# Performance work log

Measured on AMD Instinct MI355X. Metric: run time of the kernel, lower is better.

The kernel has to match this reference:

```python
import jax, jax.numpy as jnp
import numpy as np

B, H = 65536, 512


def setup_inputs() -> dict:
    key = jax.random.key(0)
    ks = jax.random.split(key, 10)
    s = 1.0 / np.sqrt(H)  # torch nn.Linear default init range
    uni = lambda k, shape: jax.random.uniform(k, shape, jnp.float32, -s, s)
    return {
        "inputs": jax.random.normal(ks[0], (B, H), jnp.float32),
        "short_term_memory": jax.random.normal(ks[1], (B, H), jnp.float32),
        "Wf": uni(ks[2], (H, H)), "bf": uni(ks[3], (H,)),
        "Wi": uni(ks[4], (H, H)), "bi": uni(ks[5], (H,)),
        "Wg": uni(ks[6], (H, H)), "bg": uni(ks[7], (H,)),
        "Wo": uni(ks[8], (H, H)), "bo": uni(ks[9], (H,)),
    }


def reference(inputs, short_term_memory, Wf, bf, Wi, bi, Wg, bg, Wo, bo):
    z = inputs + short_term_memory  # [B, H]
    # ForgetGate: OVERWRITES long-term memory (previous cell state never read).
    c = jax.nn.sigmoid(z @ Wf.T + bf)
    # InputGate: c += sigmoid(...) * tanh(...)
    c = c + jax.nn.sigmoid(z @ Wi.T + bi) * jnp.tanh(z @ Wg.T + bg)
    # OutputGate: h = tanh(c) * sigmoid(...)
    h = jnp.tanh(c) * jax.nn.sigmoid(z @ Wo.T + bo)
    return jnp.stack((c, h))  # [2, B, H]: new long-term and short-term memory
```

## Files before the change

### kernel.cpp

```cpp
#include <hip/hip_runtime.h>

typedef __bf16 bf16x8 __attribute__((ext_vector_type(8)));
typedef float  f32x4  __attribute__((ext_vector_type(4)));

#define LOG2E 1.4426950408889634f

static __device__ __forceinline__ float fexp2(float x) { return __builtin_amdgcn_exp2f(x); }
static __device__ __forceinline__ float frcp(float x)  { return __builtin_amdgcn_rcpf(x); }
static __device__ __forceinline__ float fsigmoid(float x) { return frcp(1.0f + fexp2(-LOG2E * x)); }
static __device__ __forceinline__ float ftanh(float x)    { return 2.0f * frcp(1.0f + fexp2(-2.0f * LOG2E * x)) - 1.0f; }

__global__ __launch_bounds__(256) void wpack(const float* __restrict__ Wf,
                                             const float* __restrict__ Wi,
                                             const float* __restrict__ Wg,
                                             const float* __restrict__ Wo,
                                             __bf16* __restrict__ Wp)
{
    int idx = blockIdx.x * 256 + threadIdx.x;
    int kg  = idx & 63;
    int j   = (idx >> 6) & 511;
    int g   = idx >> 15;
    const float* src = (g == 0) ? Wf : (g == 1) ? Wi : (g == 2) ? Wg : Wo;
    const float4* s4 = (const float4*)(src + j * 512 + kg * 8);
    float4 v0 = s4[0], v1 = s4[1];
    bf16x8 o;
    o[0] = (__bf16)v0.x; o[1] = (__bf16)v0.y; o[2] = (__bf16)v0.z; o[3] = (__bf16)v0.w;
    o[4] = (__bf16)v1.x; o[5] = (__bf16)v1.y; o[6] = (__bf16)v1.z; o[7] = (__bf16)v1.w;
    int cn = j >> 4;
    int ks = kg >> 2;
    int lt = (j & 15) + (kg & 3) * 16;
    size_t dst = ((size_t)(((g * 32 + cn) * 16 + ks) * 64 + lt)) * 8;
    *(bf16x8*)(Wp + dst) = o;
}

__global__ __launch_bounds__(1024, 4) void lstm_main(
    const float* __restrict__ xin, const float* __restrict__ stm,
    const __bf16* __restrict__ Wp,
    const float* __restrict__ bfv, const float* __restrict__ biv,
    const float* __restrict__ bgv, const float* __restrict__ bov,
    float* __restrict__ out)
{
    __shared__ unsigned char zs[131072];
    __shared__ unsigned char xbuf[32768];
    const int tid  = threadIdx.x;
    const int lane = tid & 63;
    const int wv   = tid >> 6;
    const int cn8  = wv & 7;
    const int rh   = wv >> 3;
    const int l15  = lane & 15;
    const int lq   = lane >> 4;
    const int row0 = blockIdx.x * 128;

    {
        const float* xb = xin + (size_t)row0 * 512;
        const float* sb = stm + (size_t)row0 * 512;
        #pragma unroll
        for (int it = 0; it < 8; ++it) {
            int idx = it * 1024 + tid;
            int row = idx >> 6;
            int kg  = idx & 63;
            const float4* x4 = (const float4*)(xb + row * 512 + kg * 8);
            const float4* s4 = (const float4*)(sb + row * 512 + kg * 8);
            float4 a0 = x4[0], a1 = x4[1];
            float4 b0 = s4[0], b1 = s4[1];
            bf16x8 p;
            p[0] = (__bf16)(a0.x + b0.x); p[1] = (__bf16)(a0.y + b0.y);
            p[2] = (__bf16)(a0.z + b0.z); p[3] = (__bf16)(a0.w + b0.w);
            p[4] = (__bf16)(a1.x + b1.x); p[5] = (__bf16)(a1.y + b1.y);
            p[6] = (__bf16)(a1.z + b1.z); p[7] = (__bf16)(a1.w + b1.w);
            int rb   = row >> 5;
            int kk   = kg >> 1;
            int slot = ((row & 31) + (kg & 1) * 32) ^ (kk & 7);
            *(bf16x8*)(zs + rb * 32768 + kk * 1024 + slot * 16) = p;
        }
    }
    __syncthreads();

    const int kkoff = lq >> 1;
    const int s0    = l15 + (lq & 1) * 32;
    const int koffb = kkoff << 10;

    const float* bias_a = rh ? bgv : bfv;
    const float* bias_b = rh ? bov : biv;

    for (int ci = 0; ci < 4; ++ci) {
        const int cn   = ci * 8 + cn8;
        const int colj = cn * 16 + l15;

        const __bf16* bpA = Wp + ((size_t)(((rh * 2    ) * 32 + cn) * 16)) * 512 + lane * 8;
        const __bf16* bpB = Wp + ((size_t)(((rh * 2 + 1) * 32 + cn) * 16)) * 512 + lane * 8;

        float biasA = bias_a[colj], biasB = bias_b[colj];
        f32x4 acc[8][2];
        #pragma unroll
        for (int m = 0; m < 8; ++m) {
            #pragma unroll
            for (int r = 0; r < 4; ++r) { acc[m][0][r] = biasA; acc[m][1][r] = biasB; }
        }

        #pragma unroll 2
        for (int ks = 0; ks < 16; ++ks) {
            const int kk7 = ((2 * ks) & 7) | kkoff;
            const int t0  = ((s0 ^ kk7) << 4) + ks * 2048 + koffb;
            bf16x8 b0 = *(const bf16x8*)(bpA + ks * 512);
            bf16x8 b1 = *(const bf16x8*)(bpB + ks * 512);
            bf16x8 a[8];
            #pragma unroll
            for (int m = 0; m < 8; ++m)
                a[m] = *(const bf16x8*)(zs + (m >> 1) * 32768 + (m & 1) * 256 + t0);
            #pragma unroll
            for (int m = 0; m < 8; ++m) {
                acc[m][0] = __builtin_amdgcn_mfma_f32_16x16x32_bf16(a[m], b0, acc[m][0], 0, 0, 0);
                acc[m][1] = __builtin_amdgcn_mfma_f32_16x16x32_bf16(a[m], b1, acc[m][1], 0, 0, 0);
            }
        }

        unsigned char* wr = xbuf + ((cn8 * 2 + rh) * 2) * 1024 + lane * 16;
        unsigned char* rd = xbuf + ((cn8 * 2 + (1 - rh)) * 2) * 1024 + lane * 16;
        #pragma unroll
        for (int mc = 0; mc < 4; ++mc) {
            __syncthreads();
            if (rh == 0) {
                *(f32x4*)(wr)        = acc[mc + 4][0];
                *(f32x4*)(wr + 1024) = acc[mc + 4][1];
            } else {
                *(f32x4*)(wr)        = acc[mc][0];
                *(f32x4*)(wr + 1024) = acc[mc][1];
            }
            __syncthreads();
            f32x4 t0v = *(const f32x4*)(rd);
            f32x4 t1v = *(const f32x4*)(rd + 1024);
            int mo = rh ? (mc + 4) : mc;
            #pragma unroll
            for (int r = 0; r < 4; ++r) {
                float F, I, G, O;
                if (rh == 0) { F = acc[mc][0][r];     I = acc[mc][1][r];     G = t0v[r]; O = t1v[r]; }
                else         { F = t0v[r]; I = t1v[r]; G = acc[mc + 4][0][r]; O = acc[mc + 4][1][r]; }
                float c = fsigmoid(F) + fsigmoid(I) * ftanh(G);
                float h = ftanh(c) * fsigmoid(O);
                int row = row0 + mo * 16 + lq * 4 + r;
                int o   = row * 512 + colj;
                out[o] = c;
                out[33554432 + o] = h;
            }
        }
    }
}

extern "C" void kernel_launch(void* const* d_in, const int* in_sizes, int n_in,
                              void* d_out, int out_size, void* d_ws, size_t ws_size,
                              hipStream_t stream) {
    const float* xin = (const float*)d_in[0];
    const float* stm = (const float*)d_in[1];
    const float* Wf  = (const float*)d_in[2];
    const float* bf_ = (const float*)d_in[3];
    const float* Wi  = (const float*)d_in[4];
    const float* bi_ = (const float*)d_in[5];
    const float* Wg  = (const float*)d_in[6];
    const float* bg_ = (const float*)d_in[7];
    const float* Wo  = (const float*)d_in[8];
    const float* bo_ = (const float*)d_in[9];
    __bf16* Wp = (__bf16*)d_ws;

    wpack<<<512, 256, 0, stream>>>(Wf, Wi, Wg, Wo, Wp);
    lstm_main<<<512, 1024, 0, stream>>>(xin, stm, Wp, bf_, bi_, bg_, bo_, (float*)d_out);
}
```

Before: 219.8 us.

## Replace block barriers with pairwise LDS flag handoff between gate-half wavefronts

Block-wide __syncthreads in the epilogue exchange are replaced by per-wave-pair producer/consumer flags in LDS. The rh=1 waves hand their G/O accumulators to the rh=0 partner through a single slot, and only rh=0 waves run the activations and stores. The packed weight layout is interleaved by gate so each wave's two B fragments sit close together, and s_setprio is raised around the MFMA block. The aim is to cut barrier stalls and let pairs progress independently, at the cost of spin-wait overhead, an unbalanced epilogue that now runs on half the waves, and subtle memory-ordering risk.

```diff
diff --git a/kernel.cpp b/kernel.cpp
--- a/kernel.cpp
+++ b/kernel.cpp
@@ -29,7 +29,7 @@
     int cn = j >> 4;
     int ks = kg >> 2;
     int lt = (j & 15) + (kg & 3) * 16;
-    size_t dst = ((size_t)(((g * 32 + cn) * 16 + ks) * 64 + lt)) * 8;
+    size_t dst = ((size_t)(((cn * 16 + ks) * 4 + g) * 64 + lt)) * 8;
     *(bf16x8*)(Wp + dst) = o;
 }
 
@@ -41,15 +41,19 @@
     float* __restrict__ out)
 {
     __shared__ unsigned char zs[131072];
-    __shared__ unsigned char xbuf[32768];
+    __shared__ unsigned char xslot[8][2048];
+    __shared__ int pf[8];
+    __shared__ int ackf[8];
     const int tid  = threadIdx.x;
     const int lane = tid & 63;
     const int wv   = tid >> 6;
-    const int cn8  = wv & 7;
+    const int p8   = wv & 7;
     const int rh   = wv >> 3;
     const int l15  = lane & 15;
     const int lq   = lane >> 4;
     const int row0 = blockIdx.x * 128;
+
+    if (tid < 8) { pf[tid] = 0; ackf[tid] = 0; }
 
     {
         const float* xb = xin + (size_t)row0 * 512;
@@ -80,17 +84,17 @@
     const int s0    = l15 + (lq & 1) * 32;
     const int koffb = kkoff << 10;
 
-    const float* bias_a = rh ? bgv : bfv;
-    const float* bias_b = rh ? bov : biv;
+    volatile int* vpf  = (volatile int*)&pf[p8];
+    volatile int* vack = (volatile int*)&ackf[p8];
+    unsigned char* slotb = &xslot[p8][0] + lane * 32;
 
     for (int ci = 0; ci < 4; ++ci) {
-        const int cn   = ci * 8 + cn8;
+        const int cn   = ci * 8 + p8;
         const int colj = cn * 16 + l15;
+        const char* wpB = (const char*)Wp + (size_t)cn * 65536 + rh * 2048 + (size_t)lane * 16;
 
-        const __bf16* bpA = Wp + ((size_t)(((rh * 2    ) * 32 + cn) * 16)) * 512 + lane * 8;
-        const __bf16* bpB = Wp + ((size_t)(((rh * 2 + 1) * 32 + cn) * 16)) * 512 + lane * 8;
-
-        float biasA = bias_a[colj], biasB = bias_b[colj];
+        float biasA = (rh ? bgv : bfv)[colj];
+        float biasB = (rh ? bov : biv)[colj];
         f32x4 acc[8][2];
         #pragma unroll
         for (int m = 0; m < 8; ++m) {
@@ -102,46 +106,52 @@
         for (int ks = 0; ks < 16; ++ks) {
             const int kk7 = ((2 * ks) & 7) | kkoff;
             const int t0  = ((s0 ^ kk7) << 4) + ks * 2048 + koffb;
-            bf16x8 b0 = *(const bf16x8*)(bpA + ks * 512);
-            bf16x8 b1 = *(const bf16x8*)(bpB + ks * 512);
+            bf16x8 b0 = *(const bf16x8*)(wpB + ks * 4096);
+            bf16x8 b1 = *(const bf16x8*)(wpB + ks * 4096 + 1024);
             bf16x8 a[8];
             #pragma unroll
             for (int m = 0; m < 8; ++m)
                 a[m] = *(const bf16x8*)(zs + (m >> 1) * 32768 + (m & 1) * 256 + t0);
+            __builtin_amdgcn_s_setprio(1);
             #pragma unroll
             for (int m = 0; m < 8; ++m) {
                 acc[m][0] = __builtin_amdgcn_mfma_f32_16x16x32_bf16(a[m], b0, acc[m][0], 0, 0, 0);
                 acc[m][1] = __builtin_amdgcn_mfma_f32_16x16x32_bf16(a[m], b1, acc[m][1], 0, 0, 0);
             }
+            __builtin_amdgcn_s_setprio(0);
         }
 
-        unsigned char* wr = xbuf + ((cn8 * 2 + rh) * 2) * 1024 + lane * 16;
-        unsigned char* rd = xbuf + ((cn8 * 2 + (1 - rh)) * 2) * 1024 + lane * 16;
-        #pragma unroll
-        for (int mc = 0; mc < 4; ++mc) {
-            __syncthreads();
-            if (rh == 0) {
-                *(f32x4*)(wr)        = acc[mc + 4][0];
-                *(f32x4*)(wr + 1024) = acc[mc + 4][1];
-            } else {
-                *(f32x4*)(wr)        = acc[mc][0];
-                *(f32x4*)(wr + 1024) = acc[mc][1];
+        if (rh == 1) {
+            #pragma unroll 1
+            for (int m = 0; m < 8; ++m) {
+                const int seq = ci * 8 + m + 1;
+                while (*vack < seq - 1) __builtin_amdgcn_s_sleep(1);
+                asm volatile("" ::: "memory");
+                *(f32x4*)(slotb)      = acc[m][0];
+                *(f32x4*)(slotb + 16) = acc[m][1];
+                asm volatile("s_waitcnt lgkmcnt(0)" ::: "memory");
+                if (lane == 0) *vpf = seq;
             }
-            __syncthreads();
-            f32x4 t0v = *(const f32x4*)(rd);
-            f32x4 t1v = *(const f32x4*)(rd + 1024);
-            int mo = rh ? (mc + 4) : mc;
-            #pragma unroll
-            for (int r = 0; r < 4; ++r) {
-                float F, I, G, O;
-                if (rh == 0) { F = acc[mc][0][r];     I = acc[mc][1][r];     G = t0v[r]; O = t1v[r]; }
-                else         { F = t0v[r]; I = t1v[r]; G = acc[mc + 4][0][r]; O = acc[mc + 4][1][r]; }
-                float c = fsigmoid(F) + fsigmoid(I) * ftanh(G);
-                float h = ftanh(c) * fsigmoid(O);
-                int row = row0 + mo * 16 + lq * 4 + r;
-                int o   = row * 512 + colj;
-                out[o] = c;
-                out[33554432 + o] = h;
+        } else {
+            #pragma unroll 1
+            for (int m = 0; m < 8; ++m) {
+                const int seq = ci * 8 + m + 1;
+                while (*vpf < seq) __builtin_amdgcn_s_sleep(1);
+                asm volatile("" ::: "memory");
+                __builtin_amdgcn_sched_barrier(0);
+                f32x4 vG = *(const f32x4*)(slotb);
+                f32x4 vO = *(const f32x4*)(slotb + 16);
+                asm volatile("s_waitcnt lgkmcnt(0)" ::: "memory");
+                if (lane == 0) *vack = seq;
+                #pragma unroll
+                for (int r = 0; r < 4; ++r) {
+                    float c = fsigmoid(acc[m][0][r]) + fsigmoid(acc[m][1][r]) * ftanh(vG[r]);
+                    float h = ftanh(c) * fsigmoid(vO[r]);
+                    int row = row0 + m * 16 + lq * 4 + r;
+                    int o   = row * 512 + colj;
+                    out[o] = c;
+                    out[33554432 + o] = h;
+                }
             }
         }
     }
```

Result: slower. 370.1 us (+68.4%).

## Software-pipeline weight loads with triple-buffered inline asm and interleaved packed layout

Applied to the files above, without the earlier changes.

Repacks the bf16 weights so that all four gates' fragments for a given column tile and k-step sit next to each other, letting each wave fetch both of its B fragments with one base address. The k-loop is fully unrolled with a three-deep register rotation of global loads issued in inline asm, gated by explicit vmcnt waits, so weight fetches overlap the MFMA work. LDS A reads are split into two halves, and MFMA groups are wrapped in setprio. The aim is to hide global load latency that previously stalled the MFMA chain. The cost is extra VGPR pressure from the buffers and fragile hand-written waitcnt sequencing.

```diff
diff --git a/kernel.cpp b/kernel.cpp
--- a/kernel.cpp
+++ b/kernel.cpp
@@ -29,7 +29,7 @@
     int cn = j >> 4;
     int ks = kg >> 2;
     int lt = (j & 15) + (kg & 3) * 16;
-    size_t dst = ((size_t)(((g * 32 + cn) * 16 + ks) * 64 + lt)) * 8;
+    size_t dst = ((size_t)(((cn * 16 + ks) * 4 + g) * 64 + lt)) * 8;
     *(bf16x8*)(Wp + dst) = o;
 }
 
@@ -45,7 +45,7 @@
     const int tid  = threadIdx.x;
     const int lane = tid & 63;
     const int wv   = tid >> 6;
-    const int cn8  = wv & 7;
+    const int p8   = wv & 7;
     const int rh   = wv >> 3;
     const int l15  = lane & 15;
     const int lq   = lane >> 4;
@@ -77,18 +77,65 @@
     __syncthreads();
 
     const int kkoff = lq >> 1;
-    const int s0    = l15 + (lq & 1) * 32;
+    const int sl0   = l15 + (lq & 1) * 32;
     const int koffb = kkoff << 10;
 
     const float* bias_a = rh ? bgv : bfv;
     const float* bias_b = rh ? bov : biv;
 
+    unsigned char* wr = xbuf + ((p8 * 2 + rh) * 2) * 1024 + lane * 16;
+    unsigned char* rd = xbuf + ((p8 * 2 + (1 - rh)) * 2) * 1024 + lane * 16;
+
+#define LOADB2(B0, B1, KS) { \
+    const char* a_ = bp + (KS) * 4096; \
+    asm volatile("global_load_dwordx4 %0, %2, off\n\t" \
+                 "global_load_dwordx4 %1, %2, off offset:1024" \
+                 : "=&v"(B0), "=&v"(B1) : "v"(a_)); }
+#define WAITB4 { asm volatile("s_waitcnt vmcnt(4)"); __builtin_amdgcn_sched_barrier(0x107); }
+#define WAITB2 { asm volatile("s_waitcnt vmcnt(2)"); __builtin_amdgcn_sched_barrier(0x107); }
+#define WAITB0 { asm volatile("s_waitcnt vmcnt(0)"); __builtin_amdgcn_sched_barrier(0x107); }
+#define DRAIN  { asm volatile("s_waitcnt vmcnt(0)"); __builtin_amdgcn_sched_barrier(0); }
+#define DOMFMA2(B0, B1, KS) { \
+    const int kk7_ = ((2 * (KS)) & 7) | kkoff; \
+    const int t0_  = ((sl0 ^ kk7_) << 4) + (KS) * 2048 + koffb; \
+    { \
+        bf16x8 a0_ = *(const bf16x8*)(zs + t0_); \
+        bf16x8 a1_ = *(const bf16x8*)(zs + t0_ + 256); \
+        bf16x8 a2_ = *(const bf16x8*)(zs + 32768 + t0_); \
+        bf16x8 a3_ = *(const bf16x8*)(zs + 32768 + t0_ + 256); \
+        __builtin_amdgcn_s_setprio(1); \
+        acc[0][0] = __builtin_amdgcn_mfma_f32_16x16x32_bf16(a0_, B0, acc[0][0], 0, 0, 0); \
+        acc[1][0] = __builtin_amdgcn_mfma_f32_16x16x32_bf16(a1_, B0, acc[1][0], 0, 0, 0); \
+        acc[2][0] = __builtin_amdgcn_mfma_f32_16x16x32_bf16(a2_, B0, acc[2][0], 0, 0, 0); \
+        acc[3][0] = __builtin_amdgcn_mfma_f32_16x16x32_bf16(a3_, B0, acc[3][0], 0, 0, 0); \
+        acc[0][1] = __builtin_amdgcn_mfma_f32_16x16x32_bf16(a0_, B1, acc[0][1], 0, 0, 0); \
+        acc[1][1] = __builtin_amdgcn_mfma_f32_16x16x32_bf16(a1_, B1, acc[1][1], 0, 0, 0); \
+        acc[2][1] = __builtin_amdgcn_mfma_f32_16x16x32_bf16(a2_, B1, acc[2][1], 0, 0, 0); \
+        acc[3][1] = __builtin_amdgcn_mfma_f32_16x16x32_bf16(a3_, B1, acc[3][1], 0, 0, 0); \
+        __builtin_amdgcn_s_setprio(0); \
+    } \
+    { \
+        bf16x8 a4_ = *(const bf16x8*)(zs + 65536 + t0_); \
+        bf16x8 a5_ = *(const bf16x8*)(zs + 65536 + t0_ + 256); \
+        bf16x8 a6_ = *(const bf16x8*)(zs + 98304 + t0_); \
+        bf16x8 a7_ = *(const bf16x8*)(zs + 98304 + t0_ + 256); \
+        __builtin_amdgcn_s_setprio(1); \
+        acc[4][0] = __builtin_amdgcn_mfma_f32_16x16x32_bf16(a4_, B0, acc[4][0], 0, 0, 0); \
+        acc[5][0] = __builtin_amdgcn_mfma_f32_16x16x32_bf16(a5_, B0, acc[5][0], 0, 0, 0); \
+        acc[6][0] = __builtin_amdgcn_mfma_f32_16x16x32_bf16(a6_, B0, acc[6][0], 0, 0, 0); \
+        acc[7][0] = __builtin_amdgcn_mfma_f32_16x16x32_bf16(a7_, B0, acc[7][0], 0, 0, 0); \
+        acc[4][1] = __builtin_amdgcn_mfma_f32_16x16x32_bf16(a4_, B1, acc[4][1], 0, 0, 0); \
+        acc[5][1] = __builtin_amdgcn_mfma_f32_16x16x32_bf16(a5_, B1, acc[5][1], 0, 0, 0); \
+        acc[6][1] = __builtin_amdgcn_mfma_f32_16x16x32_bf16(a6_, B1, acc[6][1], 0, 0, 0); \
+        acc[7][1] = __builtin_amdgcn_mfma_f32_16x16x32_bf16(a7_, B1, acc[7][1], 0, 0, 0); \
+        __builtin_amdgcn_s_setprio(0); \
+    } }
+
+    #pragma unroll 1
     for (int ci = 0; ci < 4; ++ci) {
-        const int cn   = ci * 8 + cn8;
+        const int cn   = ci * 8 + p8;
         const int colj = cn * 16 + l15;
-
-        const __bf16* bpA = Wp + ((size_t)(((rh * 2    ) * 32 + cn) * 16)) * 512 + lane * 8;
-        const __bf16* bpB = Wp + ((size_t)(((rh * 2 + 1) * 32 + cn) * 16)) * 512 + lane * 8;
+        const char* bp = (const char*)Wp + (size_t)cn * 65536 + rh * 2048 + (size_t)lane * 16;
 
         float biasA = bias_a[colj], biasB = bias_b[colj];
         f32x4 acc[8][2];
@@ -98,25 +145,33 @@
             for (int r = 0; r < 4; ++r) { acc[m][0][r] = biasA; acc[m][1][r] = biasB; }
         }
 
-        #pragma unroll 2
-        for (int ks = 0; ks < 16; ++ks) {
-            const int kk7 = ((2 * ks) & 7) | kkoff;
-            const int t0  = ((s0 ^ kk7) << 4) + ks * 2048 + koffb;
-            bf16x8 b0 = *(const bf16x8*)(bpA + ks * 512);
-            bf16x8 b1 = *(const bf16x8*)(bpB + ks * 512);
-            bf16x8 a[8];
-            #pragma unroll
-            for (int m = 0; m < 8; ++m)
-                a[m] = *(const bf16x8*)(zs + (m >> 1) * 32768 + (m & 1) * 256 + t0);
-            #pragma unroll
-            for (int m = 0; m < 8; ++m) {
-                acc[m][0] = __builtin_amdgcn_mfma_f32_16x16x32_bf16(a[m], b0, acc[m][0], 0, 0, 0);
-                acc[m][1] = __builtin_amdgcn_mfma_f32_16x16x32_bf16(a[m], b1, acc[m][1], 0, 0, 0);
-            }
-        }
-
-        unsigned char* wr = xbuf + ((cn8 * 2 + rh) * 2) * 1024 + lane * 16;
-        unsigned char* rd = xbuf + ((cn8 * 2 + (1 - rh)) * 2) * 1024 + lane * 16;
+        bf16x8 P0, P1, Q0, Q1, R0, R1;
+
+        DRAIN
+        LOADB2(P0, P1, 0)
+        LOADB2(Q0, Q1, 1)
+#define T3(KC, C0, C1, N0, N1) \
+        LOADB2(N0, N1, (KC) + 2) WAITB4 DOMFMA2(C0, C1, KC)
+        T3( 0, P0, P1, R0, R1)
+        T3( 1, Q0, Q1, P0, P1)
+        T3( 2, R0, R1, Q0, Q1)
+        T3( 3, P0, P1, R0, R1)
+        T3( 4, Q0, Q1, P0, P1)
+        T3( 5, R0, R1, Q0, Q1)
+        T3( 6, P0, P1, R0, R1)
+        T3( 7, Q0, Q1, P0, P1)
+        T3( 8, R0, R1, Q0, Q1)
+        T3( 9, P0, P1, R0, R1)
+        T3(10, Q0, Q1, P0, P1)
+        T3(11, R0, R1, Q0, Q1)
+        T3(12, P0, P1, R0, R1)
+        T3(13, Q0, Q1, P0, P1)
+#undef T3
+        WAITB2
+        DOMFMA2(R0, R1, 14)
+        WAITB0
+        DOMFMA2(P0, P1, 15)
+
         #pragma unroll
         for (int mc = 0; mc < 4; ++mc) {
             __syncthreads();
@@ -145,6 +200,12 @@
             }
         }
     }
+#undef LOADB2
+#undef WAITB4
+#undef WAITB2
+#undef WAITB0
+#undef DRAIN
+#undef DOMFMA2
 }
 
 extern "C" void kernel_launch(void* const* d_in, const int* in_sizes, int n_in,
```

Result: faster. 214.5 us (-2.4%).
